# Performance work log

Hardware: AMD Instinct MI355X
Metric: run time of the kernel (lower is better)

Reference implementation:

```python
import jax, jax.numpy as jnp
from jax import lax
import numpy as np

B, C, T = 8, 1024, 4096
H, K = 16, 7
PAD, DIL = 3, 1


def setup_inputs() -> dict:
    key = jax.random.key(0)
    k1, k2 = jax.random.split(key)
    x = jax.random.normal(k1, (B, C, T), dtype=jnp.float32)
    # xavier_uniform for weight (num_heads, 1, kernel_size)
    limit = float(np.sqrt(6.0 / (1 + K)))
    weight = jax.random.uniform(k2, (H, 1, K), dtype=jnp.float32, minval=-limit, maxval=limit)
    bias = jnp.zeros((C,), dtype=jnp.float32)
    return {"x": x, "weight": weight, "bias": bias}


def reference(x, weight, bias):
    # weight softmax over kernel taps (weight_dropout=0 at eval)
    w = jax.nn.softmax(weight, axis=-1)  # (H, 1, K)
    # torch views (B,C,T) -> (B*C/H, H, T) and runs grouped conv with groups=H,
    # so channel c uses head kernel w[c % H]. Equivalent depthwise conv with
    # the per-head kernels tiled across channels.
    kern = jnp.tile(w, (C // H, 1, 1))  # (C, 1, K), kern[c] = w[c % H]
    out = lax.conv_general_dilated(
        x, kern,
        window_strides=(1,),
        padding=[(PAD, PAD)],
        rhs_dilation=(DIL,),
        dimension_numbers=("NCH", "OIH", "NCH"),
        feature_group_count=C,
    )  # (B, C, T)
    return out + bias[None, :, None]
```

## Files before the change

### kernel.cpp

```cpp
#include <hip/hip_runtime.h>
#include <hip/hip_bf16.h>


constexpr int Bsz = 8;
constexpr int Csz = 1024;
constexpr int Tsz = 4096;
constexpr int Hsz = 16;
constexpr int Ksz = 7;
constexpr int PADsz = 3;

constexpr int TILE = 1024;
constexpr int THREADS = 256;
constexpr int TILES_PER_ROW = Tsz / TILE;

__global__ __launch_bounds__(THREADS)
void lconv1d_kernel(const float* __restrict__ x,
                    const float* __restrict__ weight,
                    const float* __restrict__ bias,
                    float* __restrict__ out) {
    __shared__ __align__(16) float lds[4 + TILE + 4];

    const int bid  = blockIdx.x;
    const int tile = bid % TILES_PER_ROW;
    const int row  = bid / TILES_PER_ROW;
    const int c    = row % Csz;
    const int h    = c % Hsz;
    const int t0   = tile * TILE;
    const int tid  = threadIdx.x;

    const float* __restrict__ xrow = x + (size_t)row * Tsz;

    {
        const float4 v = *reinterpret_cast<const float4*>(xrow + t0 + tid * 4);
        *reinterpret_cast<float4*>(&lds[4 + tid * 4]) = v;
    }
    if (tid < PADsz) {
        const int g = t0 - PADsz + tid;
        lds[1 + tid] = (g >= 0) ? xrow[g] : 0.0f;
    } else if (tid < 2 * PADsz) {
        const int j = tid - PADsz;
        const int g = t0 + TILE + j;
        lds[4 + TILE + j] = (g < Tsz) ? xrow[g] : 0.0f;
    }

    float w[Ksz];
    {
        const float* wh = weight + h * Ksz;
        float m = wh[0];
        #pragma unroll
        for (int k = 1; k < Ksz; ++k) m = fmaxf(m, wh[k]);
        float s = 0.0f;
        #pragma unroll
        for (int k = 0; k < Ksz; ++k) { w[k] = __expf(wh[k] - m); s += w[k]; }
        const float inv = 1.0f / s;
        #pragma unroll
        for (int k = 0; k < Ksz; ++k) w[k] *= inv;
    }
    const float bc = bias[c];

    __syncthreads();

    const float4 a0 = *reinterpret_cast<const float4*>(&lds[tid * 4 + 0]);
    const float4 a1 = *reinterpret_cast<const float4*>(&lds[tid * 4 + 4]);
    const float4 a2 = *reinterpret_cast<const float4*>(&lds[tid * 4 + 8]);
    float r[12] = {a0.x, a0.y, a0.z, a0.w,
                   a1.x, a1.y, a1.z, a1.w,
                   a2.x, a2.y, a2.z, a2.w};
    float4 o;
    float* op = &o.x;
    #pragma unroll
    for (int j = 0; j < 4; ++j) {
        float acc = bc;
        #pragma unroll
        for (int k = 0; k < Ksz; ++k) acc = fmaf(w[k], r[j + 1 + k], acc);
        op[j] = acc;
    }
    *reinterpret_cast<float4*>(out + (size_t)row * Tsz + t0 + tid * 4) = o;
}

extern "C" void kernel_launch(void* const* d_in, const int* in_sizes, int n_in,
                              void* d_out, int out_size, void* d_ws, size_t ws_size,
                              hipStream_t stream) {
    const float* x      = (const float*)d_in[0];
    const float* weight = (const float*)d_in[1];
    const float* bias   = (const float*)d_in[2];
    float* out          = (float*)d_out;

    const int nblocks = Bsz * Csz * TILES_PER_ROW;
    lconv1d_kernel<<<nblocks, THREADS, 0, stream>>>(x, weight, bias, out);
}
```

Measured before the change: 47.50 us.

## Drop LDS staging and load conv halos directly from global memory

Each thread now reads its own overlapping float4 neighbours straight from global memory instead of staging the tile in shared memory. This removes the LDS writes and reads and the block barrier. Each block now covers 2048 elements, with every thread processing two 1024-apart chunks, which halves the block count and keeps more loads in flight per thread. The cost is redundant global loads, which should mostly hit in cache, and edge zeroing done with multiplies. Since the kernel is already close to memory-bandwidth bound, any gain is expected to be small.

```diff
diff --git a/kernel.cpp b/kernel.cpp
--- a/kernel.cpp
+++ b/kernel.cpp
@@ -7,10 +7,10 @@
 constexpr int Tsz = 4096;
 constexpr int Hsz = 16;
 constexpr int Ksz = 7;
-constexpr int PADsz = 3;
 
-constexpr int TILE = 1024;
 constexpr int THREADS = 256;
+constexpr int TILE = 2048;
+constexpr int CHUNK = 1024;
 constexpr int TILES_PER_ROW = Tsz / TILE;
 
 __global__ __launch_bounds__(THREADS)
@@ -18,8 +18,6 @@
                     const float* __restrict__ weight,
                     const float* __restrict__ bias,
                     float* __restrict__ out) {
-    __shared__ __align__(16) float lds[4 + TILE + 4];
-
     const int bid  = blockIdx.x;
     const int tile = bid % TILES_PER_ROW;
     const int row  = bid / TILES_PER_ROW;
@@ -29,19 +27,20 @@
     const int tid  = threadIdx.x;
 
     const float* __restrict__ xrow = x + (size_t)row * Tsz;
+    float* __restrict__ orow       = out + (size_t)row * Tsz;
 
-    {
-        const float4 v = *reinterpret_cast<const float4*>(xrow + t0 + tid * 4);
-        *reinterpret_cast<float4*>(&lds[4 + tid * 4]) = v;
-    }
-    if (tid < PADsz) {
-        const int g = t0 - PADsz + tid;
-        lds[1 + tid] = (g >= 0) ? xrow[g] : 0.0f;
-    } else if (tid < 2 * PADsz) {
-        const int j = tid - PADsz;
-        const int g = t0 + TILE + j;
-        lds[4 + TILE + j] = (g < Tsz) ? xrow[g] : 0.0f;
-    }
+    const int p0 = t0 + tid * 4;
+    const int p1 = p0 + CHUNK;
+
+    const bool lA = (p0 == 0);
+    const bool rB = (p1 + 4 >= Tsz);
+
+    const float4 a0 = *reinterpret_cast<const float4*>(xrow + (lA ? p0 : p0 - 4));
+    const float4 a1 = *reinterpret_cast<const float4*>(xrow + p0);
+    const float4 a2 = *reinterpret_cast<const float4*>(xrow + p0 + 4);
+    const float4 b0 = *reinterpret_cast<const float4*>(xrow + p1 - 4);
+    const float4 b1 = *reinterpret_cast<const float4*>(xrow + p1);
+    const float4 b2 = *reinterpret_cast<const float4*>(xrow + (rB ? p1 : p1 + 4));
 
     float w[Ksz];
     {
@@ -58,24 +57,32 @@
     }
     const float bc = bias[c];
 
-    __syncthreads();
+    const float zA = lA ? 0.0f : 1.0f;
+    float ra[12] = {a0.x * zA, a0.y * zA, a0.z * zA, a0.w * zA,
+                    a1.x, a1.y, a1.z, a1.w,
+                    a2.x, a2.y, a2.z, a2.w};
+    const float zB = rB ? 0.0f : 1.0f;
+    float rb[12] = {b0.x, b0.y, b0.z, b0.w,
+                    b1.x, b1.y, b1.z, b1.w,
+                    b2.x * zB, b2.y * zB, b2.z * zB, b2.w * zB};
 
-    const float4 a0 = *reinterpret_cast<const float4*>(&lds[tid * 4 + 0]);
-    const float4 a1 = *reinterpret_cast<const float4*>(&lds[tid * 4 + 4]);
-    const float4 a2 = *reinterpret_cast<const float4*>(&lds[tid * 4 + 8]);
-    float r[12] = {a0.x, a0.y, a0.z, a0.w,
-                   a1.x, a1.y, a1.z, a1.w,
-                   a2.x, a2.y, a2.z, a2.w};
-    float4 o;
-    float* op = &o.x;
+    float4 oA, oB;
+    float* oap = &oA.x;
+    float* obp = &oB.x;
     #pragma unroll
     for (int j = 0; j < 4; ++j) {
-        float acc = bc;
+        float accA = bc, accB = bc;
         #pragma unroll
-        for (int k = 0; k < Ksz; ++k) acc = fmaf(w[k], r[j + 1 + k], acc);
-        op[j] = acc;
+        for (int k = 0; k < Ksz; ++k) {
+            accA = fmaf(w[k], ra[j + 1 + k], accA);
+            accB = fmaf(w[k], rb[j + 1 + k], accB);
+        }
+        oap[j] = accA;
+        obp[j] = accB;
     }
-    *reinterpret_cast<float4*>(out + (size_t)row * Tsz + t0 + tid * 4) = o;
+
+    *reinterpret_cast<float4*>(orow + p0) = oA;
+    *reinterpret_cast<float4*>(orow + p1) = oB;
 }
 
 extern "C" void kernel_launch(void* const* d_in, const int* in_sizes, int n_in,
```

New measurement: 44.45 us. 1.07x faster.

## Drop LDS staging, load halos directly from global, one block per row

Applied to the files above, without the earlier changes.

Removes the shared-memory tile and barrier. Each thread now reads its neighbouring float4 halos straight from global memory, relying on cache hits for the overlapping reads. Each block processes a whole row in four chunks, and outputs go out through nontemporal stores. In exchange the number of global load instructions triples and the block count drops by four, which lowers parallelism but amortises the softmax work across more outputs.

```diff
diff --git a/kernel.cpp b/kernel.cpp
--- a/kernel.cpp
+++ b/kernel.cpp
@@ -7,40 +7,34 @@
 constexpr int Tsz = 4096;
 constexpr int Hsz = 16;
 constexpr int Ksz = 7;
-constexpr int PADsz = 3;
 
-constexpr int TILE = 1024;
 constexpr int THREADS = 256;
-constexpr int TILES_PER_ROW = Tsz / TILE;
+constexpr int NCH = 4;
+
+typedef float f32x4 __attribute__((ext_vector_type(4)));
 
 __global__ __launch_bounds__(THREADS)
 void lconv1d_kernel(const float* __restrict__ x,
                     const float* __restrict__ weight,
                     const float* __restrict__ bias,
                     float* __restrict__ out) {
-    __shared__ __align__(16) float lds[4 + TILE + 4];
-
-    const int bid  = blockIdx.x;
-    const int tile = bid % TILES_PER_ROW;
-    const int row  = bid / TILES_PER_ROW;
-    const int c    = row % Csz;
-    const int h    = c % Hsz;
-    const int t0   = tile * TILE;
-    const int tid  = threadIdx.x;
+    const int row = blockIdx.x;
+    const int c   = row % Csz;
+    const int h   = c % Hsz;
+    const int tid = threadIdx.x;
 
     const float* __restrict__ xrow = x + (size_t)row * Tsz;
+    float* __restrict__ orow       = out + (size_t)row * Tsz;
 
-    {
-        const float4 v = *reinterpret_cast<const float4*>(xrow + t0 + tid * 4);
-        *reinterpret_cast<float4*>(&lds[4 + tid * 4]) = v;
-    }
-    if (tid < PADsz) {
-        const int g = t0 - PADsz + tid;
-        lds[1 + tid] = (g >= 0) ? xrow[g] : 0.0f;
-    } else if (tid < 2 * PADsz) {
-        const int j = tid - PADsz;
-        const int g = t0 + TILE + j;
-        lds[4 + TILE + j] = (g < Tsz) ? xrow[g] : 0.0f;
+    f32x4 A[NCH][3];
+    #pragma unroll
+    for (int ch = 0; ch < NCH; ++ch) {
+        const int p = tid * 4 + ch * 1024;
+        const bool lE = (p == 0);
+        const bool rE = (p + 4 >= Tsz);
+        A[ch][0] = *reinterpret_cast<const f32x4*>(xrow + (lE ? p : p - 4));
+        A[ch][1] = *reinterpret_cast<const f32x4*>(xrow + p);
+        A[ch][2] = *reinterpret_cast<const f32x4*>(xrow + (rE ? p : p + 4));
     }
 
     float w[Ksz];
@@ -58,24 +52,29 @@
     }
     const float bc = bias[c];
 
-    __syncthreads();
-
-    const float4 a0 = *reinterpret_cast<const float4*>(&lds[tid * 4 + 0]);
-    const float4 a1 = *reinterpret_cast<const float4*>(&lds[tid * 4 + 4]);
-    const float4 a2 = *reinterpret_cast<const float4*>(&lds[tid * 4 + 8]);
-    float r[12] = {a0.x, a0.y, a0.z, a0.w,
-                   a1.x, a1.y, a1.z, a1.w,
-                   a2.x, a2.y, a2.z, a2.w};
-    float4 o;
-    float* op = &o.x;
     #pragma unroll
-    for (int j = 0; j < 4; ++j) {
-        float acc = bc;
+    for (int ch = 0; ch < NCH; ++ch) {
+        const int p = tid * 4 + ch * 1024;
+        const bool lE = (p == 0);
+        const bool rE = (p + 4 >= Tsz);
+        const float zL = lE ? 0.0f : 1.0f;
+        const float zR = rE ? 0.0f : 1.0f;
+        const f32x4 a0 = A[ch][0];
+        const f32x4 a1 = A[ch][1];
+        const f32x4 a2 = A[ch][2];
+        const float r[12] = {a0.x * zL, a0.y * zL, a0.z * zL, a0.w * zL,
+                             a1.x, a1.y, a1.z, a1.w,
+                             a2.x * zR, a2.y * zR, a2.z * zR, a2.w * zR};
+        f32x4 o;
         #pragma unroll
-        for (int k = 0; k < Ksz; ++k) acc = fmaf(w[k], r[j + 1 + k], acc);
-        op[j] = acc;
+        for (int j = 0; j < 4; ++j) {
+            float acc = bc;
+            #pragma unroll
+            for (int k = 0; k < Ksz; ++k) acc = fmaf(w[k], r[j + 1 + k], acc);
+            o[j] = acc;
+        }
+        __builtin_nontemporal_store(o, reinterpret_cast<f32x4*>(orow + p));
     }
-    *reinterpret_cast<float4*>(out + (size_t)row * Tsz + t0 + tid * 4) = o;
 }
 
 extern "C" void kernel_launch(void* const* d_in, const int* in_sizes, int n_in,
@@ -86,6 +85,6 @@
     const float* bias   = (const float*)d_in[2];
     float* out          = (float*)d_out;
 
-    const int nblocks = Bsz * Csz * TILES_PER_ROW;
+    const int nblocks = Bsz * Csz;
     lconv1d_kernel<<<nblocks, THREADS, 0, stream>>>(x, weight, bias, out);
 }
```

New measurement: 43.24 us. -9.0%, faster.
